# Kernel optimization log

Measured on AMD Instinct MI355X. Metric: run time of the kernel, lower is better.

## Reference

```python
import jax, jax.numpy as jnp
import numpy as np

B, N, C, H = 4, 1024, 512, 8
HD = C // H
SCALE = HD ** -0.5
LN_EPS = 1e-5


def setup_inputs() -> dict:
    key = jax.random.key(0)
    ks = jax.random.split(key, 4)
    return {
        "x": jax.random.normal(ks[0], (B, N, C), dtype=jnp.float32),
        "Wqkv": jax.random.normal(ks[1], (C, 3 * C), dtype=jnp.float32) * (C ** -0.5),
        "bqkv": jnp.zeros((3 * C,), dtype=jnp.float32),
        "order_weights": jnp.ones((3,), dtype=jnp.float32),
        "Wproj": jax.random.normal(ks[2], (C, C), dtype=jnp.float32) * (C ** -0.5),
        "bproj": jnp.zeros((C,), dtype=jnp.float32),
        "gamma": jnp.ones((C,), dtype=jnp.float32),
        "beta": jnp.zeros((C,), dtype=jnp.float32),
    }


def reference(x, Wqkv, bqkv, order_weights, Wproj, bproj, gamma, beta):
    b, n, c = x.shape
    qkv = (x @ Wqkv + bqkv).reshape(b, n, 3, H, HD)
    qkv = jnp.transpose(qkv, (2, 0, 3, 1, 4))  # [3, B, H, N, HD]
    q, k, v = qkv[0], qkv[1], qkv[2]

    base = jnp.einsum('bhnd,bhmd->bhnm', q, k) * SCALE  # [B, H, N, N]

    ow = jax.nn.softmax(order_weights)
    # torch loop: term_0 = base, term_i = base**(i+1)
    attn = ow[0] * base
    cur = base
    for i in range(1, order_weights.shape[0]):
        cur = cur * base
        attn = attn + ow[i] * cur

    attn_final = jax.nn.softmax(attn, axis=-1)

    out = jnp.einsum('bhnm,bhmd->bhnd', attn_final, v)
    out = jnp.transpose(out, (0, 2, 1, 3)).reshape(b, n, c)
    out = out @ Wproj + bproj

    y = x + out
    mu = jnp.mean(y, axis=-1, keepdims=True)
    var = jnp.var(y, axis=-1, keepdims=True)
    y = (y - mu) / jnp.sqrt(var + LN_EPS) * gamma + beta
    return y, attn_final
```

## Files before the change

### kernel.cpp

```cpp
#include <hip/hip_runtime.h>
#include <math.h>

#define B_ 4
#define N_ 1024
#define C_ 512
#define H_ 8
#define HD_ 64
#define SCALE_ 0.125f
#define LN_EPS_ 1e-5f

typedef _Float16 f16x8 __attribute__((ext_vector_type(8)));
typedef float f32x4 __attribute__((ext_vector_type(4)));

__device__ __forceinline__ void cvt_split(const float4& A, const float4& Bv,
                                          f16x8& hi, f16x8& lo) {
    float v[8] = {A.x, A.y, A.z, A.w, Bv.x, Bv.y, Bv.z, Bv.w};
#pragma unroll
    for (int i = 0; i < 8; ++i) {
        _Float16 h = (_Float16)v[i];
        hi[i] = h;
        lo[i] = (_Float16)(v[i] - (float)h);
    }
}

__global__ __launch_bounds__(256) void wsplit_qkv(const float* __restrict__ W,
                                                  _Float16* __restrict__ wt_hi,
                                                  _Float16* __restrict__ wt_lo) {
    __shared__ float tile[64][65];
    const int tid = threadIdx.x;
    const int n0 = blockIdx.x * 64;
    const int k0 = blockIdx.y * 64;
#pragma unroll
    for (int i = 0; i < 16; ++i) {
        int e = tid + i * 256;
        int kk = e >> 6, nn = e & 63;
        tile[kk][nn] = W[(size_t)(k0 + kk) * (3 * C_) + n0 + nn];
    }
    __syncthreads();
#pragma unroll
    for (int i = 0; i < 16; ++i) {
        int e = tid + i * 256;
        int n = e >> 6, k = e & 63;
        float v = tile[k][n];
        _Float16 h = (_Float16)v;
        wt_hi[(size_t)(n0 + n) * C_ + k0 + k] = h;
        wt_lo[(size_t)(n0 + n) * C_ + k0 + k] = (_Float16)(v - (float)h);
    }
}

__global__ __launch_bounds__(256) void wsplit_proj(const float* __restrict__ W,
                                                   _Float16* __restrict__ wp_hi,
                                                   _Float16* __restrict__ wp_lo) {
    __shared__ float tile[64][65];
    const int tid = threadIdx.x;
    const int n0 = blockIdx.x * 64;
    const int k0 = blockIdx.y * 64;
#pragma unroll
    for (int i = 0; i < 16; ++i) {
        int e = tid + i * 256;
        int kk = e >> 6, nn = e & 63;
        tile[kk][nn] = W[(size_t)(k0 + kk) * C_ + n0 + nn];
    }
    __syncthreads();
#pragma unroll
    for (int i = 0; i < 16; ++i) {
        int e = tid + i * 256;
        int n = e >> 6, k = e & 63;
        float v = tile[k][n];
        _Float16 h = (_Float16)v;
        wp_hi[(size_t)(n0 + n) * C_ + k0 + k] = h;
        wp_lo[(size_t)(n0 + n) * C_ + k0 + k] = (_Float16)(v - (float)h);
    }
}

__global__ __launch_bounds__(256) void vsplit_v(const float* __restrict__ qkv,
                                                _Float16* __restrict__ vt_hi,
                                                _Float16* __restrict__ vt_lo) {
    __shared__ float tile[64][65];
    const int tid = threadIdx.x;
    const int m0 = blockIdx.x * 64;
    const int bh = blockIdx.y;
    const int b = bh >> 3, h = bh & 7;
    const size_t RS = 3 * C_;
#pragma unroll
    for (int i = 0; i < 16; ++i) {
        int e = tid + i * 256;
        int mm = e >> 6, d = e & 63;
        tile[mm][d] = qkv[(size_t)(b * N_ + m0 + mm) * RS + 2 * C_ + h * HD_ + d];
    }
    __syncthreads();
#pragma unroll
    for (int i = 0; i < 16; ++i) {
        int e = tid + i * 256;
        int d = e >> 6, mm = e & 63;
        float v = tile[mm][d];
        _Float16 hh = (_Float16)v;
        size_t idx = ((size_t)bh * HD_ + d) * N_ + m0 + mm;
        vt_hi[idx] = hh;
        vt_lo[idx] = (_Float16)(v - (float)hh);
    }
}

__global__ __launch_bounds__(256) void qkv_gemm_mfma(const float* __restrict__ x,
                                                     const _Float16* __restrict__ wt_hi,
                                                     const _Float16* __restrict__ wt_lo,
                                                     const float* __restrict__ bqkv,
                                                     float* __restrict__ qkv) {
    const int tid = threadIdx.x;
    const int lane = tid & 63;
    const int w = tid >> 6;
    const int r16 = lane & 15;
    const int g = lane >> 4;
    const int row0 = blockIdx.x * 32;
    const int col0 = blockIdx.y * 256 + w * 64;

    f32x4 acc[2][4] = {};

    const float* xr0 = x + (size_t)(row0 + r16) * C_;
    const float* xr1 = x + (size_t)(row0 + 16 + r16) * C_;

    for (int kt = 0; kt < 16; ++kt) {
        const int k0 = kt * 32 + 8 * g;
        f16x8 aHi0, aLo0, aHi1, aLo1;
        {
            float4 a0 = *(const float4*)&xr0[k0];
            float4 a1 = *(const float4*)&xr0[k0 + 4];
            cvt_split(a0, a1, aHi0, aLo0);
            float4 b0 = *(const float4*)&xr1[k0];
            float4 b1 = *(const float4*)&xr1[k0 + 4];
            cvt_split(b0, b1, aHi1, aLo1);
        }
#pragma unroll
        for (int ct = 0; ct < 4; ++ct) {
            const int c = col0 + ct * 16 + r16;
            f16x8 bHi = *(const f16x8*)&wt_hi[(size_t)c * C_ + k0];
            f16x8 bLo = *(const f16x8*)&wt_lo[(size_t)c * C_ + k0];
            acc[0][ct] = __builtin_amdgcn_mfma_f32_16x16x32_f16(aHi0, bHi, acc[0][ct], 0, 0, 0);
            acc[0][ct] = __builtin_amdgcn_mfma_f32_16x16x32_f16(aHi0, bLo, acc[0][ct], 0, 0, 0);
            acc[0][ct] = __builtin_amdgcn_mfma_f32_16x16x32_f16(aLo0, bHi, acc[0][ct], 0, 0, 0);
            acc[1][ct] = __builtin_amdgcn_mfma_f32_16x16x32_f16(aHi1, bHi, acc[1][ct], 0, 0, 0);
            acc[1][ct] = __builtin_amdgcn_mfma_f32_16x16x32_f16(aHi1, bLo, acc[1][ct], 0, 0, 0);
            acc[1][ct] = __builtin_amdgcn_mfma_f32_16x16x32_f16(aLo1, bHi, acc[1][ct], 0, 0, 0);
        }
    }

#pragma unroll
    for (int rt = 0; rt < 2; ++rt)
#pragma unroll
        for (int ct = 0; ct < 4; ++ct) {
            const int c = col0 + ct * 16 + r16;
            const float bias = bqkv[c];
#pragma unroll
            for (int j = 0; j < 4; ++j) {
                const int r = row0 + rt * 16 + 4 * g + j;
                qkv[(size_t)r * (3 * C_) + c] = acc[rt][ct][j] + bias;
            }
        }
}

__global__ __launch_bounds__(256) void attn_scores(const float* __restrict__ qkv,
                                                   const float* __restrict__ ow_in,
                                                   float* __restrict__ attn) {
    __shared__ float smax[4][16];
    __shared__ float ssum[4][16];

    const int tid = threadIdx.x;
    const int lane = tid & 63;
    const int w = tid >> 6;
    const int r16 = lane & 15;
    const int g = lane >> 4;
    const int n0 = blockIdx.x * 16;
    const int bh = blockIdx.y;
    const int b = bh >> 3, h = bh & 7;
    const size_t RS = 3 * C_;

    float w0 = ow_in[0], w1 = ow_in[1], w2 = ow_in[2];
    float wm = fmaxf(w0, fmaxf(w1, w2));
    float e0 = __expf(w0 - wm), e1 = __expf(w1 - wm), e2 = __expf(w2 - wm);
    float einv = 1.0f / (e0 + e1 + e2);
    float ow0 = e0 * einv, ow1 = e1 * einv, ow2 = e2 * einv;

    const float* qrow = qkv + (size_t)(b * N_ + n0 + r16) * RS + h * HD_;
    f16x8 aHi0, aLo0, aHi1, aLo1;
    {
        float4 qa = ((const float4*)qrow)[2 * g + 0];
        float4 qb = ((const float4*)qrow)[2 * g + 1];
        float4 qc = ((const float4*)qrow)[8 + 2 * g];
        float4 qd = ((const float4*)qrow)[9 + 2 * g];
        cvt_split(qa, qb, aHi0, aLo0);
        cvt_split(qc, qd, aHi1, aLo1);
    }

    float p[16][4];

    const float* kbase = qkv + (size_t)(b * N_) * RS + C_ + h * HD_;
#pragma unroll
    for (int t = 0; t < 16; ++t) {
        const int ct = w * 16 + t;
        const float* krow = kbase + (size_t)(ct * 16 + r16) * RS;
        float4 ka = ((const float4*)krow)[2 * g + 0];
        float4 kb = ((const float4*)krow)[2 * g + 1];
        float4 kc = ((const float4*)krow)[8 + 2 * g];
        float4 kd = ((const float4*)krow)[9 + 2 * g];
        f16x8 bHi0, bLo0, bHi1, bLo1;
        cvt_split(ka, kb, bHi0, bLo0);
        cvt_split(kc, kd, bHi1, bLo1);

        f32x4 acc = {0.f, 0.f, 0.f, 0.f};
        acc = __builtin_amdgcn_mfma_f32_16x16x32_f16(aHi0, bHi0, acc, 0, 0, 0);
        acc = __builtin_amdgcn_mfma_f32_16x16x32_f16(aHi0, bLo0, acc, 0, 0, 0);
        acc = __builtin_amdgcn_mfma_f32_16x16x32_f16(aLo0, bHi0, acc, 0, 0, 0);
        acc = __builtin_amdgcn_mfma_f32_16x16x32_f16(aHi1, bHi1, acc, 0, 0, 0);
        acc = __builtin_amdgcn_mfma_f32_16x16x32_f16(aHi1, bLo1, acc, 0, 0, 0);
        acc = __builtin_amdgcn_mfma_f32_16x16x32_f16(aLo1, bHi1, acc, 0, 0, 0);

#pragma unroll
        for (int j = 0; j < 4; ++j) {
            float s = acc[j] * SCALE_;
            p[t][j] = s * (ow0 + s * (ow1 + s * ow2));
        }
    }

    float rmax[4] = {-1e30f, -1e30f, -1e30f, -1e30f};
#pragma unroll
    for (int t = 0; t < 16; ++t)
#pragma unroll
        for (int j = 0; j < 4; ++j) rmax[j] = fmaxf(rmax[j], p[t][j]);
#pragma unroll
    for (int j = 0; j < 4; ++j)
#pragma unroll
        for (int m = 1; m < 16; m <<= 1)
            rmax[j] = fmaxf(rmax[j], __shfl_xor(rmax[j], m, 64));
    if (r16 == 0) {
#pragma unroll
        for (int j = 0; j < 4; ++j) smax[w][g * 4 + j] = rmax[j];
    }
    __syncthreads();
    float gm[4];
#pragma unroll
    for (int j = 0; j < 4; ++j) {
        int rr = g * 4 + j;
        gm[j] = fmaxf(fmaxf(smax[0][rr], smax[1][rr]),
                      fmaxf(smax[2][rr], smax[3][rr]));
    }

    float rsum[4] = {0.f, 0.f, 0.f, 0.f};
#pragma unroll
    for (int t = 0; t < 16; ++t)
#pragma unroll
        for (int j = 0; j < 4; ++j) {
            float e = __expf(p[t][j] - gm[j]);
            p[t][j] = e;
            rsum[j] += e;
        }
#pragma unroll
    for (int j = 0; j < 4; ++j)
#pragma unroll
        for (int m = 1; m < 16; m <<= 1)
            rsum[j] += __shfl_xor(rsum[j], m, 64);
    if (r16 == 0) {
#pragma unroll
        for (int j = 0; j < 4; ++j) ssum[w][g * 4 + j] = rsum[j];
    }
    __syncthreads();
    float inv[4];
#pragma unroll
    for (int j = 0; j < 4; ++j) {
        int rr = g * 4 + j;
        inv[j] = 1.0f / (ssum[0][rr] + ssum[1][rr] + ssum[2][rr] + ssum[3][rr]);
    }

    float* abase = attn + ((size_t)bh * N_ + n0 + 4 * g) * N_ + w * 256 + r16;
#pragma unroll
    for (int j = 0; j < 4; ++j) {
        float* arow = abase + (size_t)j * N_;
        float sc = inv[j];
#pragma unroll
        for (int t = 0; t < 16; ++t)
            arow[t * 16] = p[t][j] * sc;
    }
}

__global__ __launch_bounds__(256) void pv_mfma(const float* __restrict__ attn,
                                               const _Float16* __restrict__ vt_hi,
                                               const _Float16* __restrict__ vt_lo,
                                               float* __restrict__ ctx) {
    const int tid = threadIdx.x;
    const int lane = tid & 63;
    const int w = tid >> 6;
    const int r16 = lane & 15;
    const int g = lane >> 4;
    const int n0 = blockIdx.x * 64;
    const int bh = blockIdx.y;
    const int b = bh >> 3, h = bh & 7;

    const float* prow = attn + ((size_t)bh * N_ + n0 + w * 16 + r16) * N_ + 8 * g;
    const _Float16* vh = vt_hi + (size_t)bh * HD_ * N_;
    const _Float16* vl = vt_lo + (size_t)bh * HD_ * N_;

    f32x4 acc[4] = {};

    for (int kt = 0; kt < 32; kt += 4) {
        float4 p0[4], p1[4];
#pragma unroll
        for (int u = 0; u < 4; ++u) {
            const int k0 = (kt + u) * 32;
            p0[u] = *(const float4*)&prow[k0];
            p1[u] = *(const float4*)&prow[k0 + 4];
        }
#pragma unroll
        for (int u = 0; u < 4; ++u) {
            const int k0 = (kt + u) * 32 + 8 * g;
            f16x8 aHi, aLo;
            cvt_split(p0[u], p1[u], aHi, aLo);
#pragma unroll
            for (int ct = 0; ct < 4; ++ct) {
                const int d = ct * 16 + r16;
                f16x8 bHi = *(const f16x8*)&vh[(size_t)d * N_ + k0];
                f16x8 bLo = *(const f16x8*)&vl[(size_t)d * N_ + k0];
                acc[ct] = __builtin_amdgcn_mfma_f32_16x16x32_f16(aHi, bHi, acc[ct], 0, 0, 0);
                acc[ct] = __builtin_amdgcn_mfma_f32_16x16x32_f16(aHi, bLo, acc[ct], 0, 0, 0);
                acc[ct] = __builtin_amdgcn_mfma_f32_16x16x32_f16(aLo, bHi, acc[ct], 0, 0, 0);
            }
        }
    }

#pragma unroll
    for (int ct = 0; ct < 4; ++ct) {
        const int c = h * HD_ + ct * 16 + r16;
#pragma unroll
        for (int j = 0; j < 4; ++j) {
            const int r = n0 + w * 16 + 4 * g + j;
            ctx[(size_t)(b * N_ + r) * C_ + c] = acc[ct][j];
        }
    }
}

__global__ __launch_bounds__(256) void proj_mfma(const float* __restrict__ ctx,
                                                 const float* __restrict__ x,
                                                 const _Float16* __restrict__ wp_hi,
                                                 const _Float16* __restrict__ wp_lo,
                                                 const float* __restrict__ bproj,
                                                 float* __restrict__ y) {
    const int tid = threadIdx.x;
    const int lane = tid & 63;
    const int w = tid >> 6;
    const int r16 = lane & 15;
    const int g = lane >> 4;
    const int row0 = blockIdx.x * 32;
    const int colw = blockIdx.y * 128 + w * 32;

    f32x4 acc[2][2] = {};

    const float* ar0 = ctx + (size_t)(row0 + r16) * C_;
    const float* ar1 = ctx + (size_t)(row0 + 16 + r16) * C_;

    for (int kt = 0; kt < 16; kt += 2) {
        float4 a0[2], a1[2], b0[2], b1[2];
#pragma unroll
        for (int u = 0; u < 2; ++u) {
            const int k0 = (kt + u) * 32 + 8 * g;
            a0[u] = *(const float4*)&ar0[k0];
            a1[u] = *(const float4*)&ar0[k0 + 4];
            b0[u] = *(const float4*)&ar1[k0];
            b1[u] = *(const float4*)&ar1[k0 + 4];
        }
#pragma unroll
        for (int u = 0; u < 2; ++u) {
            const int k0 = (kt + u) * 32 + 8 * g;
            f16x8 aHi0, aLo0, aHi1, aLo1;
            cvt_split(a0[u], a1[u], aHi0, aLo0);
            cvt_split(b0[u], b1[u], aHi1, aLo1);
#pragma unroll
            for (int ct = 0; ct < 2; ++ct) {
                const int c = colw + ct * 16 + r16;
                f16x8 bHi = *(const f16x8*)&wp_hi[(size_t)c * C_ + k0];
                f16x8 bLo = *(const f16x8*)&wp_lo[(size_t)c * C_ + k0];
                acc[0][ct] = __builtin_amdgcn_mfma_f32_16x16x32_f16(aHi0, bHi, acc[0][ct], 0, 0, 0);
                acc[0][ct] = __builtin_amdgcn_mfma_f32_16x16x32_f16(aHi0, bLo, acc[0][ct], 0, 0, 0);
                acc[0][ct] = __builtin_amdgcn_mfma_f32_16x16x32_f16(aLo0, bHi, acc[0][ct], 0, 0, 0);
                acc[1][ct] = __builtin_amdgcn_mfma_f32_16x16x32_f16(aHi1, bHi, acc[1][ct], 0, 0, 0);
                acc[1][ct] = __builtin_amdgcn_mfma_f32_16x16x32_f16(aHi1, bLo, acc[1][ct], 0, 0, 0);
                acc[1][ct] = __builtin_amdgcn_mfma_f32_16x16x32_f16(aLo1, bHi, acc[1][ct], 0, 0, 0);
            }
        }
    }

#pragma unroll
    for (int rt = 0; rt < 2; ++rt)
#pragma unroll
        for (int ct = 0; ct < 2; ++ct) {
            const int c = colw + ct * 16 + r16;
            const float bias = bproj[c];
#pragma unroll
            for (int j = 0; j < 4; ++j) {
                const int r = row0 + rt * 16 + 4 * g + j;
                y[(size_t)r * C_ + c] = acc[rt][ct][j] + bias + x[(size_t)r * C_ + c];
            }
        }
}

__global__ __launch_bounds__(256) void ln_kernel(float* __restrict__ y,
                                                 const float* __restrict__ gamma,
                                                 const float* __restrict__ beta) {
    __shared__ float wsum[4], wsq[4];
    const int row = blockIdx.x;
    const int tid = threadIdx.x;
    const int lane = tid & 63;
    const int w = tid >> 6;

    float2 v = ((const float2*)(y + (size_t)row * C_))[tid];
    float s = v.x + v.y;
    float sq = v.x * v.x + v.y * v.y;
#pragma unroll
    for (int m = 1; m < 64; m <<= 1) {
        s += __shfl_xor(s, m, 64);
        sq += __shfl_xor(sq, m, 64);
    }
    if (lane == 0) { wsum[w] = s; wsq[w] = sq; }
    __syncthreads();
    float ts = wsum[0] + wsum[1] + wsum[2] + wsum[3];
    float tq = wsq[0] + wsq[1] + wsq[2] + wsq[3];
    float mu = ts * (1.0f / C_);
    float var = tq * (1.0f / C_) - mu * mu;
    float rstd = rsqrtf(var + LN_EPS_);

    float2 g = ((const float2*)gamma)[tid];
    float2 be = ((const float2*)beta)[tid];
    float2 o;
    o.x = (v.x - mu) * rstd * g.x + be.x;
    o.y = (v.y - mu) * rstd * g.y + be.y;
    ((float2*)(y + (size_t)row * C_))[tid] = o;
}

extern "C" void kernel_launch(void* const* d_in, const int* in_sizes, int n_in,
                              void* d_out, int out_size, void* d_ws, size_t ws_size,
                              hipStream_t stream) {
    const float* x     = (const float*)d_in[0];
    const float* Wqkv  = (const float*)d_in[1];
    const float* bqkv  = (const float*)d_in[2];
    const float* ow    = (const float*)d_in[3];
    const float* Wproj = (const float*)d_in[4];
    const float* bproj = (const float*)d_in[5];
    const float* gamma = (const float*)d_in[6];
    const float* beta  = (const float*)d_in[7];

    float* out  = (float*)d_out;
    float* y    = out;
    float* attn = out + (size_t)B_ * N_ * C_;
    float* qkv  = (float*)d_ws;
    float* ctx  = qkv + (size_t)B_ * N_ * 3 * C_;

    _Float16* wt_hi = (_Float16*)attn;
    _Float16* wt_lo = wt_hi + (size_t)(3 * C_) * C_;
    _Float16* vt_hi = (_Float16*)y;
    _Float16* vt_lo = vt_hi + (size_t)B_ * H_ * HD_ * N_;
    _Float16* wp_hi = (_Float16*)(ctx + (size_t)B_ * N_ * C_);
    _Float16* wp_lo = wp_hi + (size_t)C_ * C_;

    dim3 g0(3 * C_ / 64, C_ / 64);
    wsplit_qkv<<<g0, 256, 0, stream>>>(Wqkv, wt_hi, wt_lo);

    dim3 gp(C_ / 64, C_ / 64);
    wsplit_proj<<<gp, 256, 0, stream>>>(Wproj, wp_hi, wp_lo);

    dim3 g1(B_ * N_ / 32, 3 * C_ / 256);
    qkv_gemm_mfma<<<g1, 256, 0, stream>>>(x, wt_hi, wt_lo, bqkv, qkv);

    dim3 gv(N_ / 64, B_ * H_);
    vsplit_v<<<gv, 256, 0, stream>>>(qkv, vt_hi, vt_lo);

    dim3 g2(N_ / 16, B_ * H_);
    attn_scores<<<g2, 256, 0, stream>>>(qkv, ow, attn);

    dim3 g3(N_ / 64, B_ * H_);
    pv_mfma<<<g3, 256, 0, stream>>>(attn, vt_hi, vt_lo, ctx);

    dim3 g4(B_ * N_ / 32, C_ / 128);
    proj_mfma<<<g4, 256, 0, stream>>>(ctx, x, wp_hi, wp_lo, bproj, y);

    ln_kernel<<<B_ * N_, 256, 0, stream>>>(y, gamma, beta);
}
```

Measured before the change: 399.8 us.

## Split PV reduction dimension across warps with shared-memory reduction

```diff
diff --git a/kernel.cpp b/kernel.cpp
--- a/kernel.cpp
+++ b/kernel.cpp
@@ -285,32 +285,35 @@
                                                const _Float16* __restrict__ vt_hi,
                                                const _Float16* __restrict__ vt_lo,
                                                float* __restrict__ ctx) {
+    __shared__ float red[4][16][68];
+
     const int tid = threadIdx.x;
     const int lane = tid & 63;
     const int w = tid >> 6;
     const int r16 = lane & 15;
     const int g = lane >> 4;
-    const int n0 = blockIdx.x * 64;
+    const int n0 = blockIdx.x * 16;
     const int bh = blockIdx.y;
     const int b = bh >> 3, h = bh & 7;
 
-    const float* prow = attn + ((size_t)bh * N_ + n0 + w * 16 + r16) * N_ + 8 * g;
-    const _Float16* vh = vt_hi + (size_t)bh * HD_ * N_;
-    const _Float16* vl = vt_lo + (size_t)bh * HD_ * N_;
+    const float* prow = attn + ((size_t)bh * N_ + n0 + r16) * N_ + w * 256 + 8 * g;
+    const _Float16* vh = vt_hi + (size_t)bh * HD_ * N_ + w * 256 + 8 * g;
+    const _Float16* vl = vt_lo + (size_t)bh * HD_ * N_ + w * 256 + 8 * g;
 
     f32x4 acc[4] = {};
 
-    for (int kt = 0; kt < 32; kt += 4) {
+#pragma unroll
+    for (int grp = 0; grp < 2; ++grp) {
         float4 p0[4], p1[4];
 #pragma unroll
         for (int u = 0; u < 4; ++u) {
-            const int k0 = (kt + u) * 32;
+            const int k0 = (grp * 4 + u) * 32;
             p0[u] = *(const float4*)&prow[k0];
             p1[u] = *(const float4*)&prow[k0 + 4];
         }
 #pragma unroll
         for (int u = 0; u < 4; ++u) {
-            const int k0 = (kt + u) * 32 + 8 * g;
+            const int k0 = (grp * 4 + u) * 32;
             f16x8 aHi, aLo;
             cvt_split(p0[u], p1[u], aHi, aLo);
 #pragma unroll
@@ -326,14 +329,25 @@
     }
 
 #pragma unroll
-    for (int ct = 0; ct < 4; ++ct) {
-        const int c = h * HD_ + ct * 16 + r16;
-#pragma unroll
-        for (int j = 0; j < 4; ++j) {
-            const int r = n0 + w * 16 + 4 * g + j;
-            ctx[(size_t)(b * N_ + r) * C_ + c] = acc[ct][j];
-        }
-    }
+    for (int ct = 0; ct < 4; ++ct)
+#pragma unroll
+        for (int j = 0; j < 4; ++j)
+            red[w][4 * g + j][ct * 16 + r16] = acc[ct][j];
+    __syncthreads();
+
+    const int e = tid * 4;
+    const int row = e >> 6;
+    const int d = e & 63;
+    float4 s0 = *(const float4*)&red[0][row][d];
+    float4 s1 = *(const float4*)&red[1][row][d];
+    float4 s2 = *(const float4*)&red[2][row][d];
+    float4 s3 = *(const float4*)&red[3][row][d];
+    float4 o;
+    o.x = s0.x + s1.x + s2.x + s3.x;
+    o.y = s0.y + s1.y + s2.y + s3.y;
+    o.z = s0.z + s1.z + s2.z + s3.z;
+    o.w = s0.w + s1.w + s2.w + s3.w;
+    *(float4*)&ctx[(size_t)(b * N_ + n0 + row) * C_ + h * HD_ + d] = o;
 }
 
 __global__ __launch_bounds__(256) void proj_mfma(const float* __restrict__ ctx,
@@ -473,7 +487,7 @@
     dim3 g2(N_ / 16, B_ * H_);
     attn_scores<<<g2, 256, 0, stream>>>(qkv, ow, attn);
 
-    dim3 g3(N_ / 64, B_ * H_);
+    dim3 g3(N_ / 16, B_ * H_);
     pv_mfma<<<g3, 256, 0, stream>>>(attn, vt_hi, vt_lo, ctx);
 
     dim3 g4(B_ * N_ / 32, C_ / 128);
```

Result: no change. 399.4 us (-0.1%).
